# Optimization experiments

Measured on AMD Instinct MI355X. Metric: run time of the kernel, lower is better.

Reference implementation:

```python
import jax, jax.numpy as jnp
import numpy as np

# DAttentionBaseline config (matches init_kwargs)
NH, HC, G = 8, 32, 4          # n_heads, n_head_channels, n_groups
ORF = 2.0                      # offset_range_factor
KK = 5                         # offset conv kernel (stage_idx=2)


def _conv1x1(x, w, b=None):
    # x: (B,C,H,W), w: (O,C)
    y = jnp.einsum('bchw,oc->bohw', x, w)
    return y if b is None else y + b[None, :, None, None]


def _ref_points(Hk, Wk, dtype):
    # replicates torch.meshgrid(..., indexing='xy') as in the source
    ly = jnp.linspace(0.5, Hk - 0.5, Hk, dtype=dtype)
    lx = jnp.linspace(0.5, Wk - 0.5, Wk, dtype=dtype)
    ry, rx = jnp.meshgrid(ly, lx, indexing='xy')  # shapes (Wk, Hk); Hk==Wk here
    return jnp.stack([ry / Hk * 2 - 1, rx / Wk * 2 - 1], axis=-1)  # (Hk,Wk,2)


def _grid_sample(img, grid):
    # bilinear, align_corners=True, zero padding. img:(N,C,Hi,Wi), grid:(N,Hg,Wg,2) in [-1,1] (x,y)
    N, C, Hi, Wi = img.shape
    gx = (grid[..., 0] + 1.0) * 0.5 * (Wi - 1)
    gy = (grid[..., 1] + 1.0) * 0.5 * (Hi - 1)
    x0 = jnp.floor(gx); y0 = jnp.floor(gy)
    x1 = x0 + 1.0;      y1 = y0 + 1.0
    wx1 = gx - x0; wx0 = 1.0 - wx1
    wy1 = gy - y0; wy0 = 1.0 - wy1
    nidx = jnp.arange(N)[:, None, None]

    def gather(yf, xf):
        valid = (xf >= 0) & (xf <= Wi - 1) & (yf >= 0) & (yf <= Hi - 1)
        xi = jnp.clip(xf, 0, Wi - 1).astype(jnp.int32)
        yi = jnp.clip(yf, 0, Hi - 1).astype(jnp.int32)
        vals = img[nidx, :, yi, xi]  # (N,Hg,Wg,C)
        return vals * valid[..., None].astype(img.dtype)

    out = (gather(y0, x0) * (wy0 * wx0)[..., None]
           + gather(y0, x1) * (wy0 * wx1)[..., None]
           + gather(y1, x0) * (wy1 * wx0)[..., None]
           + gather(y1, x1) * (wy1 * wx1)[..., None])
    return out.transpose(0, 3, 1, 2)  # (N,C,Hg,Wg)


def _forward(x, wq, bq, w_off_dw, b_off_dw, ln_g, ln_b, w_off_pj, wk, bk, wv, bv, wo, bo, rpe_table):
    B, C, H, W = x.shape
    GC = C // G            # group channels
    GH = NH // G           # group heads
    scale = HC ** -0.5

    q = _conv1x1(x, wq, bq)                                   # (B,C,H,W)
    q_off = q.reshape(B * G, GC, H, W)

    # conv_offset: depthwise conv -> LayerNorm over channels -> GELU -> 1x1 conv to 2
    off = jax.lax.conv_general_dilated(
        q_off, w_off_dw, (1, 1), [(KK // 2, KK // 2), (KK // 2, KK // 2)],
        feature_group_count=GC, dimension_numbers=('NCHW', 'OIHW', 'NCHW'))
    off = off + b_off_dw[None, :, None, None]
    mu = off.mean(axis=1, keepdims=True)
    var = off.var(axis=1, keepdims=True)
    off = (off - mu) * jax.lax.rsqrt(var + 1e-5)
    off = off * ln_g[None, :, None, None] + ln_b[None, :, None, None]
    off = jax.nn.gelu(off, approximate=False)
    offset = jnp.einsum('bchw,oc->bohw', off, w_off_pj)       # (B*G,2,Hk,Wk)

    Hk, Wk = offset.shape[2], offset.shape[3]
    ns = Hk * Wk
    rng = jnp.array([1.0 / Hk, 1.0 / Wk], dtype=x.dtype).reshape(1, 2, 1, 1)
    offset = jnp.tanh(offset) * rng * ORF                     # offset_range_factor > 0
    offset = offset.transpose(0, 2, 3, 1)                     # (B*G,Hk,Wk,2)

    ref = _ref_points(Hk, Wk, x.dtype)                        # (Hk,Wk,2)
    pos = offset + ref[None]                                  # (B*G,Hk,Wk,2), (y,x) order

    xs = _grid_sample(x.reshape(B * G, GC, H, W), pos[..., ::-1])  # (B*G,GC,Hk,Wk)
    xs = xs.reshape(B, C, 1, ns)

    k = _conv1x1(xs, wk, bk).reshape(B * NH, HC, ns)
    v = _conv1x1(xs, wv, bv).reshape(B * NH, HC, ns)
    qf = q.reshape(B * NH, HC, H * W)
    attn = jnp.einsum('bcm,bcn->bmn', qf, k) * scale          # (B*NH, HW, ns)

    # RPE via grid_sample on the (2H-1, 2W-1) bias table
    rpe = jnp.broadcast_to(rpe_table[None], (B,) + rpe_table.shape)
    rpe = rpe.reshape(B * G, GH, 2 * H - 1, 2 * W - 1)
    qg = _ref_points(H, W, x.dtype).reshape(H * W, 2)
    disp = (qg[None, :, None, :] - pos.reshape(B * G, ns, 2)[:, None, :, :]) * 0.5  # (B*G,HW,ns,2)
    bias = _grid_sample(rpe, disp[..., ::-1]).reshape(B * NH, H * W, ns)
    attn = attn + bias

    attn = jax.nn.softmax(attn, axis=2)
    out = jnp.einsum('bmn,bcn->bcm', attn, v).reshape(B, C, H, W)
    y = _conv1x1(out, wo, bo)
    return (y,
            pos.reshape(B, G, Hk, Wk, 2),
            jnp.broadcast_to(ref[None, None], (B, G, Hk, Wk, 2)))


def setup_inputs() -> dict:
    key = jax.random.key(0)
    ks = jax.random.split(key, 8)
    B, C, H, W = 4, 256, 32, 32
    GC = C // G
    s = 0.02

    def n(k, shape, sc=s):
        return jax.random.normal(k, shape, jnp.float32) * sc

    return {
        'x': jax.random.normal(ks[0], (B, C, H, W), jnp.float32),
        'wq': n(ks[1], (C, C)), 'bq': jnp.zeros((C,), jnp.float32),
        'w_off_dw': n(ks[2], (GC, 1, KK, KK)), 'b_off_dw': jnp.zeros((GC,), jnp.float32),
        'ln_g': jnp.ones((GC,), jnp.float32), 'ln_b': jnp.zeros((GC,), jnp.float32),
        'w_off_pj': n(ks[3], (2, GC)),
        'wk': n(ks[4], (C, C)), 'bk': jnp.zeros((C,), jnp.float32),
        'wv': n(ks[5], (C, C)), 'bv': jnp.zeros((C,), jnp.float32),
        'wo': n(ks[6], (C, C)), 'bo': jnp.zeros((C,), jnp.float32),
        'rpe_table': n(ks[7], (NH, 2 * H - 1, 2 * W - 1), 0.01),
    }


def reference(x, wq, bq, w_off_dw, b_off_dw, ln_g, ln_b, w_off_pj, wk, bk, wv, bv, wo, bo, rpe_table):
    return _forward(x, wq, bq, w_off_dw, b_off_dw, ln_g, ln_b, w_off_pj, wk, bk, wv, bv, wo, bo, rpe_table)
```

## Files before the change

### kernel.cpp

```cpp
#include <hip/hip_runtime.h>
#include <math.h>

#define CK __restrict__

constexpr int CH = 256;
constexpr int HW = 1024;

typedef __attribute__((ext_vector_type(8))) short short8;
typedef __attribute__((ext_vector_type(4))) float f32x4;

__device__ __forceinline__ ushort f2b(float x) {
    union { float f; unsigned int u; } a; a.f = x;
    unsigned int r = (a.u + 0x7FFFu + ((a.u >> 16) & 1u)) >> 16;
    return (ushort)r;
}
__device__ __forceinline__ short8 ld8(const ushort* p) { return *(const short8*)p; }
__device__ __forceinline__ float u2f(unsigned int u) {
    union { unsigned int u; float f; } a; a.u = u; return a.f;
}

__global__ __launch_bounds__(256) void prep(const float* CK w0, const float* CK w1,
                                            const float* CK w2, const float* CK w3,
                                            ushort* CK o0, ushort* CK o1,
                                            ushort* CK o2, ushort* CK o3,
                                            const float* CK x, ushort* CK xT) {
    const int bid = blockIdx.x, t = threadIdx.x;
    if (bid < 256) {
        const float* src; ushort* dst;
        switch (bid >> 6) {
            case 0: src = w0; dst = o0; break;
            case 1: src = w1; dst = o1; break;
            case 2: src = w2; dst = o2; break;
            default: src = w3; dst = o3; break;
        }
        const int i = (bid & 63) * 256 + t;
        float4 v = ((const float4*)src)[i];
        ushort4 r; r.x = f2b(v.x); r.y = f2b(v.y); r.z = f2b(v.z); r.w = f2b(v.w);
        ((ushort4*)dst)[i] = r;
    } else {
        const int b2 = bid - 256;
        const int c8 = b2 & 31, b = b2 >> 5;
        for (int nn = 0; nn < 4; nn++) {
            const int n = nn * 256 + t;
            union { ushort u[8]; short8 s; } pk;
#pragma unroll
            for (int j = 0; j < 8; j++) pk.u[j] = f2b(x[(b * 256 + c8 * 8 + j) * HW + n]);
            *(short8*)(xT + b * 262144 + n * 256 + c8 * 8) = pk.s;
        }
    }
}

__global__ __launch_bounds__(256) void gemm_f32(const ushort* CK AT, const ushort* CK W,
                                                const float* CK bias, float* CK Y) {
    const int b = blockIdx.z;
    const int t = threadIdx.x, w = t >> 6, l = t & 63;
    const int lm = l & 15, qd = l >> 4;
    const int m0 = blockIdx.y * 64 + (w & 1) * 32;
    const int n0 = blockIdx.x * 64 + (w >> 1) * 32;
    const ushort* A = AT + b * 262144 + n0 * 256;
    const ushort* Bm = W + m0 * 256;
    f32x4 acc[2][2] = {};
#pragma unroll
    for (int k0 = 0; k0 < 8; k0++) {
        const int ko = k0 * 32 + qd * 8;
        short8 a0 = ld8(A + lm * 256 + ko);
        short8 a1 = ld8(A + (16 + lm) * 256 + ko);
        short8 b0 = ld8(Bm + lm * 256 + ko);
        short8 b1 = ld8(Bm + (16 + lm) * 256 + ko);
        acc[0][0] = __builtin_amdgcn_mfma_f32_16x16x32_bf16(a0, b0, acc[0][0], 0, 0, 0);
        acc[0][1] = __builtin_amdgcn_mfma_f32_16x16x32_bf16(a0, b1, acc[0][1], 0, 0, 0);
        acc[1][0] = __builtin_amdgcn_mfma_f32_16x16x32_bf16(a1, b0, acc[1][0], 0, 0, 0);
        acc[1][1] = __builtin_amdgcn_mfma_f32_16x16x32_bf16(a1, b1, acc[1][1], 0, 0, 0);
    }
#pragma unroll
    for (int in = 0; in < 2; in++)
#pragma unroll
        for (int im = 0; im < 2; im++) {
            const int m = m0 + im * 16 + lm;
            const float bs = bias[m];
            const int nb_ = n0 + in * 16 + qd * 4;
            float4 r;
            r.x = acc[in][im][0] + bs; r.y = acc[in][im][1] + bs;
            r.z = acc[in][im][2] + bs; r.w = acc[in][im][3] + bs;
            *(float4*)(Y + b * (CH * HW) + m * HW + nb_) = r;
        }
}

__global__ __launch_bounds__(256) void gemm_kv(const ushort* CK AT,
                                               const ushort* CK Wk, const float* CK bk, ushort* CK kbt,
                                               const ushort* CK Wv, const float* CK bv, ushort* CK vbs) {
    const int b = blockIdx.z;
    const int t = threadIdx.x, w = t >> 6, l = t & 63;
    const int lm = l & 15, qd = l >> 4;
    const int m0 = blockIdx.y * 64 + (w & 1) * 32;
    const int n0 = blockIdx.x * 64 + (w >> 1) * 32;
    const ushort* A = AT + b * 262144 + n0 * 256;
    const ushort* Bk = Wk + m0 * 256;
    const ushort* Bv = Wv + m0 * 256;
    f32x4 akT[2][2] = {}, av[2][2] = {};
#pragma unroll
    for (int k0 = 0; k0 < 8; k0++) {
        const int ko = k0 * 32 + qd * 8;
        short8 a0 = ld8(A + lm * 256 + ko);
        short8 a1 = ld8(A + (16 + lm) * 256 + ko);
        short8 k0f = ld8(Bk + lm * 256 + ko);
        short8 k1f = ld8(Bk + (16 + lm) * 256 + ko);
        short8 v0f = ld8(Bv + lm * 256 + ko);
        short8 v1f = ld8(Bv + (16 + lm) * 256 + ko);
        akT[0][0] = __builtin_amdgcn_mfma_f32_16x16x32_bf16(k0f, a0, akT[0][0], 0, 0, 0);
        akT[0][1] = __builtin_amdgcn_mfma_f32_16x16x32_bf16(k0f, a1, akT[0][1], 0, 0, 0);
        akT[1][0] = __builtin_amdgcn_mfma_f32_16x16x32_bf16(k1f, a0, akT[1][0], 0, 0, 0);
        akT[1][1] = __builtin_amdgcn_mfma_f32_16x16x32_bf16(k1f, a1, akT[1][1], 0, 0, 0);
        av[0][0] = __builtin_amdgcn_mfma_f32_16x16x32_bf16(a0, v0f, av[0][0], 0, 0, 0);
        av[0][1] = __builtin_amdgcn_mfma_f32_16x16x32_bf16(a0, v1f, av[0][1], 0, 0, 0);
        av[1][0] = __builtin_amdgcn_mfma_f32_16x16x32_bf16(a1, v0f, av[1][0], 0, 0, 0);
        av[1][1] = __builtin_amdgcn_mfma_f32_16x16x32_bf16(a1, v1f, av[1][1], 0, 0, 0);
    }
#pragma unroll
    for (int im = 0; im < 2; im++)
#pragma unroll
        for (int in = 0; in < 2; in++) {
            {
                const int c0 = m0 + im * 16 + qd * 4;
                const int n  = n0 + in * 16 + lm;
                const int nh = c0 >> 5, ch = c0 & 31;
                const int bh = b * 8 + nh;
                const int qdk = ch >> 3, co4 = ch & 7;
                const int nc = n >> 7, nbk = (n >> 4) & 7, lmk = n & 15;
                const float4 bks = *(const float4*)(bk + c0);
                ushort4 r4;
                r4.x = f2b(akT[im][in][0] + bks.x);
                r4.y = f2b(akT[im][in][1] + bks.y);
                r4.z = f2b(akT[im][in][2] + bks.z);
                r4.w = f2b(akT[im][in][3] + bks.w);
                *(ushort4*)(kbt + ((bh * 8 + nc) * 512 + nbk * 64 + qdk * 16 + lmk) * 8 + co4) = r4;
            }
            {
                const int c = m0 + im * 16 + lm;
                const int nh = c >> 5, ch = c & 31;
                const int bh = b * 8 + nh;
                const float bs = bv[c];
                const int cb = (ch >> 4) & 1, lmv = ch & 15;
                const int nbase = n0 + in * 16 + qd * 4;
                const int nc = nbase >> 7, kc = (nbase >> 5) & 3;
                const int qdv = (nbase >> 3) & 3, co0 = nbase & 7;
                ushort4 r4;
                r4.x = f2b(av[in][im][0] + bs); r4.y = f2b(av[in][im][1] + bs);
                r4.z = f2b(av[in][im][2] + bs); r4.w = f2b(av[in][im][3] + bs);
                *(ushort4*)(vbs + ((bh * 8 + nc) * 512 + (cb * 4 + kc) * 64 + qdv * 16 + lmv) * 8 + co0) = r4;
            }
        }
}

__global__ __launch_bounds__(256) void dwconv(const float* CK q, const float* CK wdw,
                                              const float* CK bdw, float* CK off) {
    const int bx = blockIdx.x;
    const int ch = bx & 63;
    const float* qb = q + bx * HW;
    float w[25];
#pragma unroll
    for (int i = 0; i < 25; i++) w[i] = wdw[ch * 25 + i];
    const float bb = bdw[ch];
    const int t = threadIdx.x;
#pragma unroll
    for (int p = 0; p < 4; p++) {
        int hw = p * 256 + t;
        int ii = hw >> 5, jj = hw & 31;
        float s = bb;
#pragma unroll
        for (int ky = 0; ky < 5; ky++) {
            int y = ii + ky - 2;
            if (y < 0 || y > 31) continue;
#pragma unroll
            for (int kx = 0; kx < 5; kx++) {
                int x = jj + kx - 2;
                if (x < 0 || x > 31) continue;
                s += qb[y * 32 + x] * w[ky * 5 + kx];
            }
        }
        off[bx * HW + hw] = s;
    }
}

__global__ __launch_bounds__(64) void ln_pos_sample(const float* CK off, const float* CK ln_g,
                                                    const float* CK ln_b, const float* CK wpj,
                                                    const float* CK x,
                                                    float* CK pos_ws, float* CK out_pos,
                                                    float* CK out_ref, ushort* CK xsT) {
    const int bg = blockIdx.x >> 4;
    const int n = (blockIdx.x & 15) * 64 + threadIdx.x;
    const int gid = bg * 1024 + n;
    const float* ob = off + bg * 64 * HW + n;
    float s1 = 0.f;
#pragma unroll
    for (int c = 0; c < 64; c++) s1 += ob[c * HW];
    const float mean = s1 * 0.015625f;
    float s2 = 0.f;
#pragma unroll
    for (int c = 0; c < 64; c++) { float d = ob[c * HW] - mean; s2 += d * d; }
    const float rs = rsqrtf(s2 * 0.015625f + 1e-5f);
    float p0a = 0.f, p1a = 0.f;
#pragma unroll
    for (int c = 0; c < 64; c++) {
        float vv = (ob[c * HW] - mean) * rs * ln_g[c] + ln_b[c];
        float gl = 0.5f * vv * (1.f + erff(vv * 0.70710678118654752f));
        p0a += gl * wpj[c];
        p1a += gl * wpj[64 + c];
    }
    const int ii = n >> 5, jj = n & 31;
    const float r0 = (jj + 0.5f) * 0.0625f - 1.f;
    const float r1 = (ii + 0.5f) * 0.0625f - 1.f;
    const float pos0 = tanhf(p0a) * 0.0625f + r0;
    const float pos1 = tanhf(p1a) * 0.0625f + r1;
    pos_ws[gid * 2] = pos0;  pos_ws[gid * 2 + 1] = pos1;
    out_pos[gid * 2] = pos0; out_pos[gid * 2 + 1] = pos1;
    out_ref[gid * 2] = r0;   out_ref[gid * 2 + 1] = r1;

    const float gx = (pos1 + 1.f) * 15.5f, gy = (pos0 + 1.f) * 15.5f;
    const float x0f = floorf(gx), y0f = floorf(gy);
    const float wx1 = gx - x0f, wx0 = 1.f - wx1, wy1 = gy - y0f, wy0 = 1.f - wy1;
    const bool vx0 = (x0f >= 0.f) && (x0f <= 31.f);
    const bool vx1 = (x0f >= -1.f) && (x0f <= 30.f);
    const bool vy0 = (y0f >= 0.f) && (y0f <= 31.f);
    const bool vy1 = (y0f >= -1.f) && (y0f <= 30.f);
    const int xi0 = (int)fminf(fmaxf(x0f, 0.f), 31.f);
    const int xi1 = (int)fminf(fmaxf(x0f + 1.f, 0.f), 31.f);
    const int yi0 = (int)fminf(fmaxf(y0f, 0.f), 31.f);
    const int yi1 = (int)fminf(fmaxf(y0f + 1.f, 0.f), 31.f);
    const float w00 = (vy0 && vx0) ? wy0 * wx0 : 0.f;
    const float w01 = (vy0 && vx1) ? wy0 * wx1 : 0.f;
    const float w10 = (vy1 && vx0) ? wy1 * wx0 : 0.f;
    const float w11 = (vy1 && vx1) ? wy1 * wx1 : 0.f;
    const int o00 = yi0 * 32 + xi0, o01 = yi0 * 32 + xi1;
    const int o10 = yi1 * 32 + xi0, o11 = yi1 * 32 + xi1;
    const int b = bg >> 2, g = bg & 3;
    const float* xb = x + bg * 64 * HW;
    ushort* xo = xsT + b * 262144 + n * 256 + g * 64;
#pragma unroll
    for (int c4 = 0; c4 < 16; c4++) {
        ushort4 r4;
        float vals[4];
#pragma unroll
        for (int j = 0; j < 4; j++) {
            const float* p = xb + (c4 * 4 + j) * HW;
            vals[j] = w00 * p[o00] + w01 * p[o01] + w10 * p[o10] + w11 * p[o11];
        }
        r4.x = f2b(vals[0]); r4.y = f2b(vals[1]); r4.z = f2b(vals[2]); r4.w = f2b(vals[3]);
        *(ushort4*)(xo + c4 * 4) = r4;
    }
}

__global__ __launch_bounds__(256) void attn_mfma(const float* CK q, const ushort* CK kbt,
                                                 const ushort* CK vbs, const float* CK pos_ws,
                                                 const float* CK rpe, ushort* CK aoT) {
    __shared__ __align__(16) unsigned int rpe_pr[65 * 66];
    __shared__ __align__(16) ushort ksb[4096];
    __shared__ __align__(16) ushort vsb[4096];
    __shared__ __align__(16) ushort Pl[4][2176];
    __shared__ __align__(16) float2 poss2[128];
    const int bh = blockIdx.y;
    const int b = bh >> 3, nh = bh & 7, bg = bh >> 1;
    const int t = threadIdx.x;
    const int w = t >> 6, l = t & 63;
    const int lm = l & 15, qd = l >> 4;

    {
        const float* rp = rpe + nh * 3969;
        for (int i = t; i < 65 * 66; i += 256) {
            int y = i / 66, x = i - y * 66;
            int yy = y - 1, xx = x - 1;
            bool vy = (yy >= 0) && (yy < 63);
            float a  = (vy && xx >= 0 && xx < 63) ? rp[yy * 63 + xx] : 0.f;
            float bb = (vy && xx + 1 >= 0 && xx + 1 < 63) ? rp[yy * 63 + xx + 1] : 0.f;
            rpe_pr[i] = (unsigned int)f2b(a) | ((unsigned int)f2b(bb) << 16);
        }
    }

    const int m = blockIdx.x * 64 + w * 16 + lm;
    short8 qf;
    {
        union { ushort u[8]; short8 s; } pk;
        const float* qb = q + (b * 256 + nh * 32) * HW + m;
#pragma unroll
        for (int j = 0; j < 8; j++) pk.u[j] = f2b(qb[(qd * 8 + j) * HW]);
        qf = pk.s;
    }
    const float qg0 = ((m & 31) + 0.5f) * 0.0625f - 1.f;
    const float qg1 = ((m >> 5) + 0.5f) * 0.0625f - 1.f;
    const float ax = 31.f + 15.5f * qg1;
    const float ay = 31.f + 15.5f * qg0;

    f32x4 oacc0 = {0.f, 0.f, 0.f, 0.f}, oacc1 = {0.f, 0.f, 0.f, 0.f};
    float rmax = -3e38f, rsum = 0.f;
    ushort* PlW = Pl[w];

    for (int nc = 0; nc < 8; nc++) {
        __syncthreads();
        {
            const int4* ksrc = (const int4*)(kbt + (bh * 8 + nc) * 4096);
            int4* kdst = (int4*)ksb;
            kdst[t] = ksrc[t]; kdst[t + 256] = ksrc[t + 256];
            const int4* vsrc = (const int4*)(vbs + (bh * 8 + nc) * 4096);
            int4* vdst = (int4*)vsb;
            vdst[t] = vsrc[t]; vdst[t + 256] = vsrc[t + 256];
            if (t < 128) {
                float2 pp = ((const float2*)pos_ws)[bg * 1024 + nc * 128 + t];
                poss2[t].x = pp.x * 15.5f; poss2[t].y = pp.y * 15.5f;
            }
        }
        __syncthreads();

        f32x4 sT[8];
#pragma unroll
        for (int nb = 0; nb < 8; nb++) {
            short8 kf = ld8(ksb + (nb * 64 + l) * 8);
            sT[nb] = __builtin_amdgcn_mfma_f32_16x16x32_bf16(kf, qf,
                        (f32x4){0.f, 0.f, 0.f, 0.f}, 0, 0, 0);
        }

        float cmax = -3e38f;
#pragma unroll
        for (int nb = 0; nb < 8; nb++) {
            const float4* pp = (const float4*)&poss2[nb * 16 + qd * 4];
            const float4 pa = pp[0], pb_ = pp[1];
            const float psx[4] = {pa.x, pa.z, pb_.x, pb_.z};
            const float psy[4] = {pa.y, pa.w, pb_.y, pb_.w};
#pragma unroll
            for (int r = 0; r < 4; r++) {
                const float gx = ax - psy[r];
                const float gy = ay - psx[r];
                const float x0f = floorf(gx), y0f = floorf(gy);
                const float wx1 = gx - x0f, wy1 = gy - y0f;
                const int idx = (int)y0f * 66 + (int)x0f + 67;
                const unsigned int pr0 = rpe_pr[idx];
                const unsigned int pr1 = rpe_pr[idx + 66];
                const float t00 = u2f(pr0 << 16), t01 = u2f(pr0 & 0xFFFF0000u);
                const float t10 = u2f(pr1 << 16), t11 = u2f(pr1 & 0xFFFF0000u);
                const float u0 = t00 + wx1 * (t01 - t00);
                const float u1 = t10 + wx1 * (t11 - t10);
                const float bias = u0 + wy1 * (u1 - u0);
                sT[nb][r] = sT[nb][r] * 0.17677669529663687f + bias;
                cmax = fmaxf(cmax, sT[nb][r]);
            }
        }
        cmax = fmaxf(cmax, __shfl_xor(cmax, 16));
        cmax = fmaxf(cmax, __shfl_xor(cmax, 32));
        const float newmax = fmaxf(rmax, cmax);
        const float alpha = __expf(rmax - newmax);
        rmax = newmax;

        float csum = 0.f;
#pragma unroll
        for (int nb = 0; nb < 8; nb++) {
            float e0 = __expf(sT[nb][0] - rmax);
            float e1 = __expf(sT[nb][1] - rmax);
            float e2 = __expf(sT[nb][2] - rmax);
            float e3 = __expf(sT[nb][3] - rmax);
            csum += (e0 + e1) + (e2 + e3);
            uint2 pk;
            pk.x = (unsigned int)f2b(e0) | ((unsigned int)f2b(e1) << 16);
            pk.y = (unsigned int)f2b(e2) | ((unsigned int)f2b(e3) << 16);
            *(uint2*)(PlW + nb * 272 + l * 4) = pk;
        }
        csum += __shfl_xor(csum, 16);
        csum += __shfl_xor(csum, 32);
        rsum = rsum * alpha + csum;
        oacc0 *= alpha;
        oacc1 *= alpha;

#pragma unroll
        for (int kc = 0; kc < 4; kc++) {
            const ushort* pb2 = PlW + (kc * 2 + (qd >> 1)) * 272 + (qd & 1) * 128 + lm * 4;
            union { uint2 u[2]; short8 s; } pfu;
            pfu.u[0] = *(const uint2*)pb2;
            pfu.u[1] = *(const uint2*)(pb2 + 64);
            short8 vf0 = ld8(vsb + (kc * 64 + l) * 8);
            short8 vf1 = ld8(vsb + ((4 + kc) * 64 + l) * 8);
            oacc0 = __builtin_amdgcn_mfma_f32_16x16x32_bf16(vf0, pfu.s, oacc0, 0, 0, 0);
            oacc1 = __builtin_amdgcn_mfma_f32_16x16x32_bf16(vf1, pfu.s, oacc1, 0, 0, 0);
        }
    }

    const float inv = 1.f / rsum;
    ushort* ob = aoT + b * 262144 + m * 256 + nh * 32 + qd * 4;
    ushort4 r04, r14;
    r04.x = f2b(oacc0[0] * inv); r04.y = f2b(oacc0[1] * inv);
    r04.z = f2b(oacc0[2] * inv); r04.w = f2b(oacc0[3] * inv);
    r14.x = f2b(oacc1[0] * inv); r14.y = f2b(oacc1[1] * inv);
    r14.z = f2b(oacc1[2] * inv); r14.w = f2b(oacc1[3] * inv);
    *(ushort4*)ob = r04;
    *(ushort4*)(ob + 16) = r14;
}

extern "C" void kernel_launch(void* const* d_in, const int* in_sizes, int n_in,
                              void* d_out, int out_size, void* d_ws, size_t ws_size,
                              hipStream_t stream) {
    (void)in_sizes; (void)n_in; (void)out_size; (void)ws_size;
    const float* x   = (const float*)d_in[0];
    const float* wq  = (const float*)d_in[1];
    const float* bq  = (const float*)d_in[2];
    const float* wdw = (const float*)d_in[3];
    const float* bdw = (const float*)d_in[4];
    const float* lng = (const float*)d_in[5];
    const float* lnb = (const float*)d_in[6];
    const float* wpj = (const float*)d_in[7];
    const float* wk  = (const float*)d_in[8];
    const float* bk  = (const float*)d_in[9];
    const float* wv  = (const float*)d_in[10];
    const float* bv  = (const float*)d_in[11];
    const float* wo  = (const float*)d_in[12];
    const float* bo  = (const float*)d_in[13];
    const float* rpe = (const float*)d_in[14];
    float* outp = (float*)d_out;
    char* base = (char*)d_ws;
    const size_t MB = 1 << 20;

    float*  q_ws   = (float*)(base);
    float*  off_ws = (float*)(base + 4 * MB);
    float*  pos_ws = (float*)(base + 8 * MB);
    ushort* xT     = (ushort*)(base + 8 * MB + 131072);
    ushort* xsT    = (ushort*)(base + 10 * MB + 131072);
    ushort* kbt    = (ushort*)(base + 12 * MB + 131072);
    ushort* vbs    = (ushort*)(base + 14 * MB + 131072);
    ushort* aoT    = (ushort*)(base + 16 * MB + 131072);
    ushort* wqb    = (ushort*)(base + 18 * MB + 131072);
    ushort* wkb    = (ushort*)(base + 18 * MB + 262144);
    ushort* wvb    = (ushort*)(base + 18 * MB + 393216);
    ushort* wob    = (ushort*)(base + 18 * MB + 524288);

    prep<<<384, 256, 0, stream>>>(wq, wk, wv, wo, wqb, wkb, wvb, wob, x, xT);
    gemm_f32<<<dim3(16, 4, 4), 256, 0, stream>>>(xT, wqb, bq, q_ws);
    dwconv<<<1024, 256, 0, stream>>>(q_ws, wdw, bdw, off_ws);
    ln_pos_sample<<<256, 64, 0, stream>>>(off_ws, lng, lnb, wpj, x, pos_ws,
                                          outp + (1 << 20), outp + (1 << 20) + 32768, xsT);
    gemm_kv<<<dim3(16, 4, 4), 256, 0, stream>>>(xsT, wkb, bk, kbt, wvb, bv, vbs);
    attn_mfma<<<dim3(16, 32), 256, 0, stream>>>(q_ws, kbt, vbs, pos_ws, rpe, aoT);
    gemm_f32<<<dim3(16, 4, 4), 256, 0, stream>>>(aoT, wob, bo, outp);
}
```

Before: 194.7 us.

## Split attention over key halves, shrink GEMM tiles, precompute RPE table, widen LN kernel

```diff
diff --git a/kernel.cpp b/kernel.cpp
--- a/kernel.cpp
+++ b/kernel.cpp
@@ -18,12 +18,14 @@
 __device__ __forceinline__ float u2f(unsigned int u) {
     union { unsigned int u; float f; } a; a.u = u; return a.f;
 }
+__device__ __forceinline__ float b2f(ushort us) { return u2f((unsigned int)us << 16); }
 
 __global__ __launch_bounds__(256) void prep(const float* CK w0, const float* CK w1,
                                             const float* CK w2, const float* CK w3,
                                             ushort* CK o0, ushort* CK o1,
                                             ushort* CK o2, ushort* CK o3,
-                                            const float* CK x, ushort* CK xT) {
+                                            const float* CK x, ushort* CK xT,
+                                            const float* CK rpe, unsigned int* CK rpetab) {
     const int bid = blockIdx.x, t = threadIdx.x;
     if (bid < 256) {
         const float* src; ushort* dst;
@@ -37,7 +39,7 @@
         float4 v = ((const float4*)src)[i];
         ushort4 r; r.x = f2b(v.x); r.y = f2b(v.y); r.z = f2b(v.z); r.w = f2b(v.w);
         ((ushort4*)dst)[i] = r;
-    } else {
+    } else if (bid < 384) {
         const int b2 = bid - 256;
         const int c8 = b2 & 31, b = b2 >> 5;
         for (int nn = 0; nn < 4; nn++) {
@@ -47,6 +49,18 @@
             for (int j = 0; j < 8; j++) pk.u[j] = f2b(x[(b * 256 + c8 * 8 + j) * HW + n]);
             *(short8*)(xT + b * 262144 + n * 256 + c8 * 8) = pk.s;
         }
+    } else {
+        const int h = bid - 384;
+        const float* rp = rpe + h * 3969;
+        unsigned int* dst = rpetab + h * 4356;
+        for (int i = t; i < 4356; i += 256) {
+            int y = i / 67, x2 = i - y * 67;
+            int yy = y - 1, xx = x2 - 1;
+            bool vy = (yy >= 0) && (yy < 63) && (y < 65);
+            float a  = (vy && xx >= 0 && xx < 63) ? rp[yy * 63 + xx] : 0.f;
+            float bb = (vy && xx >= -1 && xx < 62) ? rp[yy * 63 + xx + 1] : 0.f;
+            dst[i] = (unsigned int)f2b(a) | ((unsigned int)f2b(bb) << 16);
+        }
     }
 }
 
@@ -55,35 +69,20 @@
     const int b = blockIdx.z;
     const int t = threadIdx.x, w = t >> 6, l = t & 63;
     const int lm = l & 15, qd = l >> 4;
-    const int m0 = blockIdx.y * 64 + (w & 1) * 32;
-    const int n0 = blockIdx.x * 64 + (w >> 1) * 32;
-    const ushort* A = AT + b * 262144 + n0 * 256;
-    const ushort* Bm = W + m0 * 256;
-    f32x4 acc[2][2] = {};
+    const int m0 = blockIdx.y * 16;
+    const int np = blockIdx.x * 64 + w * 16;
+    const ushort* A  = AT + b * 262144 + (np + lm) * 256;
+    const ushort* Bm = W + (m0 + lm) * 256;
+    f32x4 acc = {0.f, 0.f, 0.f, 0.f};
 #pragma unroll
     for (int k0 = 0; k0 < 8; k0++) {
         const int ko = k0 * 32 + qd * 8;
-        short8 a0 = ld8(A + lm * 256 + ko);
-        short8 a1 = ld8(A + (16 + lm) * 256 + ko);
-        short8 b0 = ld8(Bm + lm * 256 + ko);
-        short8 b1 = ld8(Bm + (16 + lm) * 256 + ko);
-        acc[0][0] = __builtin_amdgcn_mfma_f32_16x16x32_bf16(a0, b0, acc[0][0], 0, 0, 0);
-        acc[0][1] = __builtin_amdgcn_mfma_f32_16x16x32_bf16(a0, b1, acc[0][1], 0, 0, 0);
-        acc[1][0] = __builtin_amdgcn_mfma_f32_16x16x32_bf16(a1, b0, acc[1][0], 0, 0, 0);
-        acc[1][1] = __builtin_amdgcn_mfma_f32_16x16x32_bf16(a1, b1, acc[1][1], 0, 0, 0);
-    }
-#pragma unroll
-    for (int in = 0; in < 2; in++)
-#pragma unroll
-        for (int im = 0; im < 2; im++) {
-            const int m = m0 + im * 16 + lm;
-            const float bs = bias[m];
-            const int nb_ = n0 + in * 16 + qd * 4;
-            float4 r;
-            r.x = acc[in][im][0] + bs; r.y = acc[in][im][1] + bs;
-            r.z = acc[in][im][2] + bs; r.w = acc[in][im][3] + bs;
-            *(float4*)(Y + b * (CH * HW) + m * HW + nb_) = r;
-        }
+        acc = __builtin_amdgcn_mfma_f32_16x16x32_bf16(ld8(A + ko), ld8(Bm + ko), acc, 0, 0, 0);
+    }
+    const float bs = bias[m0 + lm];
+    float4 r;
+    r.x = acc[0] + bs; r.y = acc[1] + bs; r.z = acc[2] + bs; r.w = acc[3] + bs;
+    *(float4*)(Y + b * 262144 + (m0 + lm) * HW + np + qd * 4) = r;
 }
 
 __global__ __launch_bounds__(256) void gemm_kv(const ushort* CK AT,
@@ -92,64 +91,44 @@
     const int b = blockIdx.z;
     const int t = threadIdx.x, w = t >> 6, l = t & 63;
     const int lm = l & 15, qd = l >> 4;
-    const int m0 = blockIdx.y * 64 + (w & 1) * 32;
-    const int n0 = blockIdx.x * 64 + (w >> 1) * 32;
-    const ushort* A = AT + b * 262144 + n0 * 256;
-    const ushort* Bk = Wk + m0 * 256;
-    const ushort* Bv = Wv + m0 * 256;
-    f32x4 akT[2][2] = {}, av[2][2] = {};
+    const int m0 = blockIdx.y * 16;
+    const int np = blockIdx.x * 64 + w * 16;
+    const ushort* A  = AT + b * 262144 + (np + lm) * 256;
+    const ushort* Kw = Wk + (m0 + lm) * 256;
+    const ushort* Vw = Wv + (m0 + lm) * 256;
+    f32x4 akT = {0.f, 0.f, 0.f, 0.f}, av = {0.f, 0.f, 0.f, 0.f};
 #pragma unroll
     for (int k0 = 0; k0 < 8; k0++) {
         const int ko = k0 * 32 + qd * 8;
-        short8 a0 = ld8(A + lm * 256 + ko);
-        short8 a1 = ld8(A + (16 + lm) * 256 + ko);
-        short8 k0f = ld8(Bk + lm * 256 + ko);
-        short8 k1f = ld8(Bk + (16 + lm) * 256 + ko);
-        short8 v0f = ld8(Bv + lm * 256 + ko);
-        short8 v1f = ld8(Bv + (16 + lm) * 256 + ko);
-        akT[0][0] = __builtin_amdgcn_mfma_f32_16x16x32_bf16(k0f, a0, akT[0][0], 0, 0, 0);
-        akT[0][1] = __builtin_amdgcn_mfma_f32_16x16x32_bf16(k0f, a1, akT[0][1], 0, 0, 0);
-        akT[1][0] = __builtin_amdgcn_mfma_f32_16x16x32_bf16(k1f, a0, akT[1][0], 0, 0, 0);
-        akT[1][1] = __builtin_amdgcn_mfma_f32_16x16x32_bf16(k1f, a1, akT[1][1], 0, 0, 0);
-        av[0][0] = __builtin_amdgcn_mfma_f32_16x16x32_bf16(a0, v0f, av[0][0], 0, 0, 0);
-        av[0][1] = __builtin_amdgcn_mfma_f32_16x16x32_bf16(a0, v1f, av[0][1], 0, 0, 0);
-        av[1][0] = __builtin_amdgcn_mfma_f32_16x16x32_bf16(a1, v0f, av[1][0], 0, 0, 0);
-        av[1][1] = __builtin_amdgcn_mfma_f32_16x16x32_bf16(a1, v1f, av[1][1], 0, 0, 0);
-    }
-#pragma unroll
-    for (int im = 0; im < 2; im++)
-#pragma unroll
-        for (int in = 0; in < 2; in++) {
-            {
-                const int c0 = m0 + im * 16 + qd * 4;
-                const int n  = n0 + in * 16 + lm;
-                const int nh = c0 >> 5, ch = c0 & 31;
-                const int bh = b * 8 + nh;
-                const int qdk = ch >> 3, co4 = ch & 7;
-                const int nc = n >> 7, nbk = (n >> 4) & 7, lmk = n & 15;
-                const float4 bks = *(const float4*)(bk + c0);
-                ushort4 r4;
-                r4.x = f2b(akT[im][in][0] + bks.x);
-                r4.y = f2b(akT[im][in][1] + bks.y);
-                r4.z = f2b(akT[im][in][2] + bks.z);
-                r4.w = f2b(akT[im][in][3] + bks.w);
-                *(ushort4*)(kbt + ((bh * 8 + nc) * 512 + nbk * 64 + qdk * 16 + lmk) * 8 + co4) = r4;
-            }
-            {
-                const int c = m0 + im * 16 + lm;
-                const int nh = c >> 5, ch = c & 31;
-                const int bh = b * 8 + nh;
-                const float bs = bv[c];
-                const int cb = (ch >> 4) & 1, lmv = ch & 15;
-                const int nbase = n0 + in * 16 + qd * 4;
-                const int nc = nbase >> 7, kc = (nbase >> 5) & 3;
-                const int qdv = (nbase >> 3) & 3, co0 = nbase & 7;
-                ushort4 r4;
-                r4.x = f2b(av[in][im][0] + bs); r4.y = f2b(av[in][im][1] + bs);
-                r4.z = f2b(av[in][im][2] + bs); r4.w = f2b(av[in][im][3] + bs);
-                *(ushort4*)(vbs + ((bh * 8 + nc) * 512 + (cb * 4 + kc) * 64 + qdv * 16 + lmv) * 8 + co0) = r4;
-            }
-        }
+        short8 a = ld8(A + ko);
+        akT = __builtin_amdgcn_mfma_f32_16x16x32_bf16(ld8(Kw + ko), a, akT, 0, 0, 0);
+        av  = __builtin_amdgcn_mfma_f32_16x16x32_bf16(a, ld8(Vw + ko), av, 0, 0, 0);
+    }
+    {
+        const int ch0 = m0 + qd * 4;
+        const int pix = np + lm;
+        const int bh = b * 8 + (ch0 >> 5);
+        const int qdk = (ch0 & 31) >> 3, co4 = ch0 & 7;
+        const int nc = pix >> 7, nbk = (pix >> 4) & 7, lmk = pix & 15;
+        const float4 bks = *(const float4*)(bk + ch0);
+        ushort4 r4;
+        r4.x = f2b(akT[0] + bks.x); r4.y = f2b(akT[1] + bks.y);
+        r4.z = f2b(akT[2] + bks.z); r4.w = f2b(akT[3] + bks.w);
+        *(ushort4*)(kbt + ((bh * 8 + nc) * 512 + nbk * 64 + qdk * 16 + lmk) * 8 + co4) = r4;
+    }
+    {
+        const int ch = m0 + lm;
+        const int pix0 = np + qd * 4;
+        const int bh = b * 8 + (ch >> 5);
+        const int cb = (ch & 31) >> 4, lmv = ch & 15;
+        const int nc = pix0 >> 7, kc = (pix0 >> 5) & 3;
+        const int qdv = (pix0 >> 3) & 3, co0 = pix0 & 7;
+        const float bs = bv[ch];
+        ushort4 r4;
+        r4.x = f2b(av[0] + bs); r4.y = f2b(av[1] + bs);
+        r4.z = f2b(av[2] + bs); r4.w = f2b(av[3] + bs);
+        *(ushort4*)(vbs + ((bh * 8 + nc) * 512 + (cb * 4 + kc) * 64 + qdv * 16 + lmv) * 8 + co0) = r4;
+    }
 }
 
 __global__ __launch_bounds__(256) void dwconv(const float* CK q, const float* CK wdw,
@@ -182,40 +161,48 @@
     }
 }
 
-__global__ __launch_bounds__(64) void ln_pos_sample(const float* CK off, const float* CK ln_g,
-                                                    const float* CK ln_b, const float* CK wpj,
-                                                    const float* CK x,
-                                                    float* CK pos_ws, float* CK out_pos,
-                                                    float* CK out_ref, ushort* CK xsT) {
-    const int bg = blockIdx.x >> 4;
-    const int n = (blockIdx.x & 15) * 64 + threadIdx.x;
+__global__ __launch_bounds__(256) void lnps(const float* CK off, const float* CK ln_g,
+                                            const float* CK ln_b, const float* CK wpj,
+                                            const float* CK x,
+                                            float* CK out_pos, float* CK out_ref,
+                                            float2* CK pos_sc, ushort* CK xsT) {
+    const int bid = blockIdx.x, t = threadIdx.x;
+    const int bg = bid >> 4;
+    const int pix_l = t >> 2, qtr = t & 3;
+    const int n = (bid & 15) * 64 + pix_l;
     const int gid = bg * 1024 + n;
     const float* ob = off + bg * 64 * HW + n;
+    const int c0 = qtr * 16;
     float s1 = 0.f;
 #pragma unroll
-    for (int c = 0; c < 64; c++) s1 += ob[c * HW];
+    for (int j = 0; j < 16; j++) s1 += ob[(c0 + j) * HW];
+    s1 += __shfl_xor(s1, 1); s1 += __shfl_xor(s1, 2);
     const float mean = s1 * 0.015625f;
     float s2 = 0.f;
 #pragma unroll
-    for (int c = 0; c < 64; c++) { float d = ob[c * HW] - mean; s2 += d * d; }
+    for (int j = 0; j < 16; j++) { float d = ob[(c0 + j) * HW] - mean; s2 += d * d; }
+    s2 += __shfl_xor(s2, 1); s2 += __shfl_xor(s2, 2);
     const float rs = rsqrtf(s2 * 0.015625f + 1e-5f);
-    float p0a = 0.f, p1a = 0.f;
-#pragma unroll
-    for (int c = 0; c < 64; c++) {
-        float vv = (ob[c * HW] - mean) * rs * ln_g[c] + ln_b[c];
+    float p0 = 0.f, p1 = 0.f;
+#pragma unroll
+    for (int j = 0; j < 16; j++) {
+        float vv = (ob[(c0 + j) * HW] - mean) * rs * ln_g[c0 + j] + ln_b[c0 + j];
         float gl = 0.5f * vv * (1.f + erff(vv * 0.70710678118654752f));
-        p0a += gl * wpj[c];
-        p1a += gl * wpj[64 + c];
-    }
+        p0 += gl * wpj[c0 + j];
+        p1 += gl * wpj[64 + c0 + j];
+    }
+    p0 += __shfl_xor(p0, 1); p0 += __shfl_xor(p0, 2);
+    p1 += __shfl_xor(p1, 1); p1 += __shfl_xor(p1, 2);
     const int ii = n >> 5, jj = n & 31;
     const float r0 = (jj + 0.5f) * 0.0625f - 1.f;
     const float r1 = (ii + 0.5f) * 0.0625f - 1.f;
-    const float pos0 = tanhf(p0a) * 0.0625f + r0;
-    const float pos1 = tanhf(p1a) * 0.0625f + r1;
-    pos_ws[gid * 2] = pos0;  pos_ws[gid * 2 + 1] = pos1;
-    out_pos[gid * 2] = pos0; out_pos[gid * 2 + 1] = pos1;
-    out_ref[gid * 2] = r0;   out_ref[gid * 2 + 1] = r1;
-
+    const float pos0 = tanhf(p0) * 0.0625f + r0;
+    const float pos1 = tanhf(p1) * 0.0625f + r1;
+    if (qtr == 0) {
+        out_pos[gid * 2] = pos0; out_pos[gid * 2 + 1] = pos1;
+        out_ref[gid * 2] = r0;   out_ref[gid * 2 + 1] = r1;
+        pos_sc[gid].x = pos0 * 15.5f; pos_sc[gid].y = pos1 * 15.5f;
+    }
     const float gx = (pos1 + 1.f) * 15.5f, gy = (pos0 + 1.f) * 15.5f;
     const float x0f = floorf(gx), y0f = floorf(gy);
     const float wx1 = gx - x0f, wx0 = 1.f - wx1, wy1 = gy - y0f, wy0 = 1.f - wy1;
@@ -235,46 +222,39 @@
     const int o10 = yi1 * 32 + xi0, o11 = yi1 * 32 + xi1;
     const int b = bg >> 2, g = bg & 3;
     const float* xb = x + bg * 64 * HW;
-    ushort* xo = xsT + b * 262144 + n * 256 + g * 64;
-#pragma unroll
-    for (int c4 = 0; c4 < 16; c4++) {
+    ushort* xo = xsT + b * 262144 + n * 256 + g * 64 + c0;
+#pragma unroll
+    for (int j4 = 0; j4 < 4; j4++) {
         ushort4 r4;
         float vals[4];
 #pragma unroll
         for (int j = 0; j < 4; j++) {
-            const float* p = xb + (c4 * 4 + j) * HW;
+            const float* p = xb + (c0 + j4 * 4 + j) * HW;
             vals[j] = w00 * p[o00] + w01 * p[o01] + w10 * p[o10] + w11 * p[o11];
         }
         r4.x = f2b(vals[0]); r4.y = f2b(vals[1]); r4.z = f2b(vals[2]); r4.w = f2b(vals[3]);
-        *(ushort4*)(xo + c4 * 4) = r4;
-    }
-}
-
-__global__ __launch_bounds__(256) void attn_mfma(const float* CK q, const ushort* CK kbt,
-                                                 const ushort* CK vbs, const float* CK pos_ws,
-                                                 const float* CK rpe, ushort* CK aoT) {
-    __shared__ __align__(16) unsigned int rpe_pr[65 * 66];
-    __shared__ __align__(16) ushort ksb[4096];
-    __shared__ __align__(16) ushort vsb[4096];
+        *(ushort4*)(xo + j4 * 4) = r4;
+    }
+}
+
+__global__ __launch_bounds__(256, 4) void attn_part(const float* CK q, const ushort* CK kbt,
+                                                    const ushort* CK vbs, const float2* CK pos_sc,
+                                                    const unsigned int* CK rpetab,
+                                                    ushort* CK partO, float2* CK mlbuf) {
+    __shared__ __align__(16) unsigned int rpe_pr[4356];
     __shared__ __align__(16) ushort Pl[4][2176];
-    __shared__ __align__(16) float2 poss2[128];
-    const int bh = blockIdx.y;
+    const int bh = blockIdx.y, half = blockIdx.z;
     const int b = bh >> 3, nh = bh & 7, bg = bh >> 1;
     const int t = threadIdx.x;
     const int w = t >> 6, l = t & 63;
     const int lm = l & 15, qd = l >> 4;
 
     {
-        const float* rp = rpe + nh * 3969;
-        for (int i = t; i < 65 * 66; i += 256) {
-            int y = i / 66, x = i - y * 66;
-            int yy = y - 1, xx = x - 1;
-            bool vy = (yy >= 0) && (yy < 63);
-            float a  = (vy && xx >= 0 && xx < 63) ? rp[yy * 63 + xx] : 0.f;
-            float bb = (vy && xx + 1 >= 0 && xx + 1 < 63) ? rp[yy * 63 + xx + 1] : 0.f;
-            rpe_pr[i] = (unsigned int)f2b(a) | ((unsigned int)f2b(bb) << 16);
-        }
-    }
+        const uint4* src4 = (const uint4*)(rpetab + nh * 4356);
+        uint4* dst4 = (uint4*)rpe_pr;
+        for (int i = t; i < 1089; i += 256) dst4[i] = src4[i];
+    }
+    __syncthreads();
 
     const int m = blockIdx.x * 64 + w * 16 + lm;
     short8 qf;
@@ -293,35 +273,23 @@
     f32x4 oacc0 = {0.f, 0.f, 0.f, 0.f}, oacc1 = {0.f, 0.f, 0.f, 0.f};
     float rmax = -3e38f, rsum = 0.f;
     ushort* PlW = Pl[w];
-
-    for (int nc = 0; nc < 8; nc++) {
-        __syncthreads();
-        {
-            const int4* ksrc = (const int4*)(kbt + (bh * 8 + nc) * 4096);
-            int4* kdst = (int4*)ksb;
-            kdst[t] = ksrc[t]; kdst[t + 256] = ksrc[t + 256];
-            const int4* vsrc = (const int4*)(vbs + (bh * 8 + nc) * 4096);
-            int4* vdst = (int4*)vsb;
-            vdst[t] = vsrc[t]; vdst[t + 256] = vsrc[t + 256];
-            if (t < 128) {
-                float2 pp = ((const float2*)pos_ws)[bg * 1024 + nc * 128 + t];
-                poss2[t].x = pp.x * 15.5f; poss2[t].y = pp.y * 15.5f;
-            }
-        }
-        __syncthreads();
+    const float2* pbase = pos_sc + bg * 1024;
+
+    for (int nc = half * 4; nc < half * 4 + 4; nc++) {
+        const ushort* kg = kbt + (bh * 8 + nc) * 4096;
+        const ushort* vg = vbs + (bh * 8 + nc) * 4096;
 
         f32x4 sT[8];
 #pragma unroll
         for (int nb = 0; nb < 8; nb++) {
-            short8 kf = ld8(ksb + (nb * 64 + l) * 8);
-            sT[nb] = __builtin_amdgcn_mfma_f32_16x16x32_bf16(kf, qf,
+            sT[nb] = __builtin_amdgcn_mfma_f32_16x16x32_bf16(ld8(kg + (nb * 64 + l) * 8), qf,
                         (f32x4){0.f, 0.f, 0.f, 0.f}, 0, 0, 0);
         }
 
         float cmax = -3e38f;
 #pragma unroll
         for (int nb = 0; nb < 8; nb++) {
-            const float4* pp = (const float4*)&poss2[nb * 16 + qd * 4];
+            const float4* pp = (const float4*)(pbase + nc * 128 + nb * 16 + qd * 4);
             const float4 pa = pp[0], pb_ = pp[1];
             const float psx[4] = {pa.x, pa.z, pb_.x, pb_.z};
             const float psy[4] = {pa.y, pa.w, pb_.y, pb_.w};
@@ -331,9 +299,9 @@
                 const float gy = ay - psx[r];
                 const float x0f = floorf(gx), y0f = floorf(gy);
                 const float wx1 = gx - x0f, wy1 = gy - y0f;
-                const int idx = (int)y0f * 66 + (int)x0f + 67;
+                const int idx = (int)y0f * 67 + (int)x0f + 68;
                 const unsigned int pr0 = rpe_pr[idx];
-                const unsigned int pr1 = rpe_pr[idx + 66];
+                const unsigned int pr1 = rpe_pr[idx + 67];
                 const float t00 = u2f(pr0 << 16), t01 = u2f(pr0 & 0xFFFF0000u);
                 const float t10 = u2f(pr1 << 16), t11 = u2f(pr1 & 0xFFFF0000u);
                 const float u0 = t00 + wx1 * (t01 - t00);
@@ -374,22 +342,53 @@
             union { uint2 u[2]; short8 s; } pfu;
             pfu.u[0] = *(const uint2*)pb2;
             pfu.u[1] = *(const uint2*)(pb2 + 64);
-            short8 vf0 = ld8(vsb + (kc * 64 + l) * 8);
-            short8 vf1 = ld8(vsb + ((4 + kc) * 64 + l) * 8);
-            oacc0 = __builtin_amdgcn_mfma_f32_16x16x32_bf16(vf0, pfu.s, oacc0, 0, 0, 0);
-            oacc1 = __builtin_amdgcn_mfma_f32_16x16x32_bf16(vf1, pfu.s, oacc1, 0, 0, 0);
-        }
-    }
-
-    const float inv = 1.f / rsum;
-    ushort* ob = aoT + b * 262144 + m * 256 + nh * 32 + qd * 4;
+            oacc0 = __builtin_amdgcn_mfma_f32_16x16x32_bf16(ld8(vg + (kc * 64 + l) * 8), pfu.s, oacc0, 0, 0, 0);
+            oacc1 = __builtin_amdgcn_mfma_f32_16x16x32_bf16(ld8(vg + ((4 + kc) * 64 + l) * 8), pfu.s, oacc1, 0, 0, 0);
+        }
+    }
+
+    ushort* po = partO + (((half * 32 + bh) * 1024 + m) * 32) + qd * 4;
     ushort4 r04, r14;
-    r04.x = f2b(oacc0[0] * inv); r04.y = f2b(oacc0[1] * inv);
-    r04.z = f2b(oacc0[2] * inv); r04.w = f2b(oacc0[3] * inv);
-    r14.x = f2b(oacc1[0] * inv); r14.y = f2b(oacc1[1] * inv);
-    r14.z = f2b(oacc1[2] * inv); r14.w = f2b(oacc1[3] * inv);
-    *(ushort4*)ob = r04;
-    *(ushort4*)(ob + 16) = r14;
+    r04.x = f2b(oacc0[0]); r04.y = f2b(oacc0[1]); r04.z = f2b(oacc0[2]); r04.w = f2b(oacc0[3]);
+    r14.x = f2b(oacc1[0]); r14.y = f2b(oacc1[1]); r14.z = f2b(oacc1[2]); r14.w = f2b(oacc1[3]);
+    *(ushort4*)po = r04;
+    *(ushort4*)(po + 16) = r14;
+    if (qd == 0) {
+        float2 ml; ml.x = rmax; ml.y = rsum;
+        mlbuf[(half * 32 + bh) * 1024 + m] = ml;
+    }
+}
+
+__global__ __launch_bounds__(256) void attn_comb(const ushort* CK partO, const float2* CK mlbuf,
+                                                 ushort* CK aoT) {
+    const int gid = blockIdx.x * 256 + threadIdx.x;
+    const int bh = gid >> 10, m = gid & 1023;
+    const int b = bh >> 3, nh = bh & 7;
+    const float2 ml0 = mlbuf[bh * 1024 + m];
+    const float2 ml1 = mlbuf[(32 + bh) * 1024 + m];
+    const float M = fmaxf(ml0.x, ml1.x);
+    const float e0 = __expf(ml0.x - M), e1 = __expf(ml1.x - M);
+    const float inv = 1.f / (ml0.y * e0 + ml1.y * e1);
+    const float w0 = e0 * inv, w1 = e1 * inv;
+    const ushort* p0 = partO + (bh * 1024 + m) * 32;
+    const ushort* p1 = partO + ((32 + bh) * 1024 + m) * 32;
+    ushort* ob = aoT + b * 262144 + m * 256 + nh * 32;
+#pragma unroll
+    for (int h = 0; h < 2; h++) {
+        union { ushort u[8]; short8 s; } a, c, o;
+        a.s = ld8(p0 + h * 8 + (h >> 1) * 0);
+        a.s = ld8(p0 + h * 16);
+        c.s = ld8(p1 + h * 16);
+#pragma unroll
+        for (int j = 0; j < 8; j++) o.u[j] = f2b(b2f(a.u[j]) * w0 + b2f(c.u[j]) * w1);
+        *(short8*)(ob + h * 16) = o.s;
+        union { ushort u[8]; short8 s; } a2, c2, o2;
+        a2.s = ld8(p0 + h * 16 + 8);
+        c2.s = ld8(p1 + h * 16 + 8);
+#pragma unroll
+        for (int j = 0; j < 8; j++) o2.u[j] = f2b(b2f(a2.u[j]) * w0 + b2f(c2.u[j]) * w1);
+        *(short8*)(ob + h * 16 + 8) = o2.s;
+    }
 }
 
 extern "C" void kernel_launch(void* const* d_in, const int* in_sizes, int n_in,
@@ -417,8 +416,10 @@
 
     float*  q_ws   = (float*)(base);
     float*  off_ws = (float*)(base + 4 * MB);
-    float*  pos_ws = (float*)(base + 8 * MB);
+    ushort* partO  = (ushort*)(base + 4 * MB);
+    float2* pos_sc = (float2*)(base + 8 * MB);
     ushort* xT     = (ushort*)(base + 8 * MB + 131072);
+    float2* mlbuf  = (float2*)(base + 8 * MB + 131072);
     ushort* xsT    = (ushort*)(base + 10 * MB + 131072);
     ushort* kbt    = (ushort*)(base + 12 * MB + 131072);
     ushort* vbs    = (ushort*)(base + 14 * MB + 131072);
@@ -427,13 +428,15 @@
     ushort* wkb    = (ushort*)(base + 18 * MB + 262144);
     ushort* wvb    = (ushort*)(base + 18 * MB + 393216);
     ushort* wob    = (ushort*)(base + 18 * MB + 524288);
-
-    prep<<<384, 256, 0, stream>>>(wq, wk, wv, wo, wqb, wkb, wvb, wob, x, xT);
-    gemm_f32<<<dim3(16, 4, 4), 256, 0, stream>>>(xT, wqb, bq, q_ws);
+    unsigned int* rpetab = (unsigned int*)(base + 18 * MB + 655360);
+
+    prep<<<392, 256, 0, stream>>>(wq, wk, wv, wo, wqb, wkb, wvb, wob, x, xT, rpe, rpetab);
+    gemm_f32<<<dim3(16, 16, 4), 256, 0, stream>>>(xT, wqb, bq, q_ws);
     dwconv<<<1024, 256, 0, stream>>>(q_ws, wdw, bdw, off_ws);
-    ln_pos_sample<<<256, 64, 0, stream>>>(off_ws, lng, lnb, wpj, x, pos_ws,
-                                          outp + (1 << 20), outp + (1 << 20) + 32768, xsT);
-    gemm_kv<<<dim3(16, 4, 4), 256, 0, stream>>>(xsT, wkb, bk, kbt, wvb, bv, vbs);
-    attn_mfma<<<dim3(16, 32), 256, 0, stream>>>(q_ws, kbt, vbs, pos_ws, rpe, aoT);
-    gemm_f32<<<dim3(16, 4, 4), 256, 0, stream>>>(aoT, wob, bo, outp);
-}
+    lnps<<<256, 256, 0, stream>>>(off_ws, lng, lnb, wpj, x,
+                                  outp + (1 << 20), outp + (1 << 20) + 32768, pos_sc, xsT);
+    gemm_kv<<<dim3(16, 16, 4), 256, 0, stream>>>(xsT, wkb, bk, kbt, wvb, bv, vbs);
+    attn_part<<<dim3(16, 32, 2), 256, 0, stream>>>(q_ws, kbt, vbs, pos_sc, rpetab, partO, mlbuf);
+    attn_comb<<<128, 256, 0, stream>>>(partO, mlbuf, aoT);
+    gemm_f32<<<dim3(16, 16, 4), 256, 0, stream>>>(aoT, wob, bo, outp);
+}
```

After: 202.8 us. 4.2% more time.
